# Kernel tuning notes

Hardware: AMD Instinct MI355X
Metric: run time of the kernel (lower is better)

## Reference

```python
import jax, jax.numpy as jnp
import numpy as np

# Module constants (from init_kwargs)
ANCHORS = np.array([[116.0, 90.0], [156.0, 198.0], [373.0, 326.0]], dtype=np.float32)
ANCHOR_AREAS = jnp.asarray(ANCHORS[:, 0] * ANCHORS[:, 1])  # [A]
A, H, W, C = 3, 128, 128, 2
IMG_W, IMG_H = 1024.0, 1024.0
STRIDE_W, STRIDE_H = IMG_W / H, IMG_H / W
ATTRS = 5 + C
LAMBDA_XY, LAMBDA_WH, LAMBDA_CONF, LAMBDA_CLS = 2.5, 2.5, 1.0, 1.0


def setup_inputs() -> dict:
    key = jax.random.key(0)
    k1, k2, k3, k4, k5 = jax.random.split(key, 5)
    B, T = 64, 2
    # conf/class feed BCELoss -> predictions must lie in [0,1)
    output = jax.random.uniform(k1, (B, A * H * W * ATTRS), dtype=jnp.float32)
    # Corner-format target boxes constructed so the (buggy) cell index
    # int((w - cx)/stride) is always within [0, mapSize).
    x1 = jax.random.uniform(k2, (B, T), minval=0.0, maxval=20.0)
    y1 = jax.random.uniform(k3, (B, T), minval=0.0, maxval=20.0)
    x2 = x1 + jax.random.uniform(k4, (B, T), minval=200.0, maxval=880.0)
    y2 = y1 + jax.random.uniform(k5, (B, T), minval=200.0, maxval=880.0)
    boxes = jnp.stack([x1, y1, x2, y2], axis=-1)  # [B,T,4]
    areas = (x2 - x1) * (y2 - y1)                 # [B,T]
    labels = jnp.ones((B, T), dtype=jnp.int32)    # label 1 -> valid for both one-hot quirks
    return {"output": output, "boxes": boxes, "labels": labels, "areas": areas}


def _bce(p, t):
    # torch BCELoss: mean, with log clamped to -100
    lp = jnp.maximum(jnp.log(p), -100.0)
    l1p = jnp.maximum(jnp.log1p(-p), -100.0)
    return -jnp.mean(t * lp + (1.0 - t) * l1p)


def _mse(p, t):
    return jnp.mean((p - t) ** 2)


def yolo_loss(output, boxes, labels, areas):
    B = output.shape[0]
    T = boxes.shape[1]
    out = output.reshape(B, A, H, W, ATTRS)
    x, y, w, h, conf = out[..., 0], out[..., 1], out[..., 2], out[..., 3], out[..., 4]
    cls = out[..., 5:]  # [B,A,H,W,C]

    gx = jnp.arange(H, dtype=output.dtype)[None, None, :, None]  # xCoord axis
    gy = jnp.arange(W, dtype=output.dtype)[None, None, None, :]  # yCoord axis
    x = x - gx
    y = y - gy

    # convert target boxes corners -> center format (done in-place in the original)
    cx = (boxes[..., 0] + boxes[..., 2]) * 0.5
    cy = (boxes[..., 1] + boxes[..., 3]) * 0.5
    bw = boxes[..., 2] - boxes[..., 0]
    bh = boxes[..., 3] - boxes[..., 1]
    tb = jnp.stack([cx, cy, bw, bh], axis=-1)  # [B,T,4]

    # class one-hots: target 0 uses labels[0]; targets i>=1 use labels[i]-1 (original quirk)
    cls0 = jax.nn.one_hot(labels[:, 0], C, dtype=output.dtype)
    cls1 = jax.nn.one_hot(labels[:, 1] - 1, C, dtype=output.dtype)
    tcls = jnp.stack([cls0, cls1], axis=1)            # [B,T,C]
    full = jnp.concatenate([tb, tcls], axis=-1)       # [B,T,4+C]

    best_anchor = jnp.argmin(jnp.abs(ANCHOR_AREAS[None, None, :] - areas[..., None]), axis=-1)  # [B,T]
    # original computes cell as int((w - cx)/stride), int((h - cy)/stride)
    cellX = ((bw - cx) / STRIDE_W).astype(jnp.int32)
    cellY = ((bh - cy) / STRIDE_H).astype(jnp.int32)

    mask = jnp.zeros((B, A, H, W), jnp.int32)
    exact = jnp.zeros((B, A, H, W), bool)
    bidx = jnp.arange(B)
    for i in range(T):  # tiny fixed loop over targets; later targets overwrite, as in torch
        mask = mask.at[bidx, best_anchor[:, i], cellX[:, i], cellY[:, i]].set(i)
        exact = exact.at[bidx, best_anchor[:, i], cellX[:, i], cellY[:, i]].set(True)

    matched = full[bidx[:, None, None, None], mask]  # [B,A,H,W,4+C]

    zero = jnp.zeros((), output.dtype)
    tX = jnp.where(exact, matched[..., 0] - gx, zero)
    tY = jnp.where(exact, matched[..., 1] - gy, zero)
    tW = jnp.where(exact, matched[..., 2], zero)
    tH = jnp.where(exact, matched[..., 3], zero)
    tConf = exact.astype(output.dtype)
    # targetMatched[5:] has length C-1==1 and broadcasts to all C slots (original quirk)
    tCls = jnp.where(exact[..., None], jnp.broadcast_to(matched[..., 5:6], cls.shape), zero)

    # IOU: prediction (x-gx, y-gy, w, h) converted center->corners; target center-format
    # boxes are (incorrectly, but faithfully) treated as corners.
    px1, py1 = x - w * 0.5, y - h * 0.5
    px2, py2 = x + w * 0.5, y + h * 0.5
    tx1 = tb[..., 0][:, None, None, None, :]  # [B,1,1,1,T]
    ty1 = tb[..., 1][:, None, None, None, :]
    tx2 = tb[..., 2][:, None, None, None, :]
    ty2 = tb[..., 3][:, None, None, None, :]
    ix = jnp.clip(jnp.minimum(px2[..., None], tx2) - jnp.maximum(px1[..., None], tx1), 0.0)
    iy = jnp.clip(jnp.minimum(py2[..., None], ty2) - jnp.maximum(py1[..., None], ty1), 0.0)
    inter = ix * iy                                   # [B,A,H,W,T]
    area_p = (px2 - px1) * (py2 - py1)                # [B,A,H,W]
    area_t = ((tx2 - tx1) * (ty2 - ty1))              # [B,1,1,1,T]
    iou = inter / (area_p[..., None] + area_t - inter + 1e-16)
    max_iou = jnp.max(iou, axis=-1)                   # [B,A,H,W]

    suppress = jnp.logical_and(~exact, max_iou > 0.5)
    xf = jnp.where(exact, x, zero)
    yf = jnp.where(exact, y, zero)
    wf = jnp.where(exact, w, zero)
    hf = jnp.where(exact, h, zero)
    clsf = jnp.where(exact[..., None], cls, zero)
    conff = jnp.where(suppress, zero, conf)

    xL, yL = _mse(xf, tX), _mse(yf, tY)
    wL, hL = _mse(wf, tW), _mse(hf, tH)
    confL = _bce(conff, tConf)
    clsL = _bce(clsf, tCls)
    loss = (xL + yL) * LAMBDA_XY + (wL + hL) * LAMBDA_WH + confL * LAMBDA_CONF + clsL * LAMBDA_CLS
    return (loss, xL, yL, wL, hL, confL, clsL)


def reference(output, boxes, labels, areas):
    return yolo_loss(output, boxes, labels, areas)
```

## Files before the change

### kernel.cpp

```cpp
#include <hip/hip_runtime.h>
#include <math.h>

#define A_ 3
#define H_ 128
#define W_ 128
#define C_ 2
#define ATTRS 7
#define B_ 64
#define CELLS_PER_BATCH (A_*H_*W_)
#define TOTAL_CELLS (B_*CELLS_PER_BATCH)

#define NTHR 256
#define CPT 4
#define CELLS_PER_BLOCK (NTHR*CPT)
#define NBLK (TOTAL_CELLS/CELLS_PER_BLOCK)

__global__ __launch_bounds__(NTHR) void yolo_main_k(
    const float* __restrict__ outp,
    const float* __restrict__ boxes,
    const int*   __restrict__ labels,
    const float* __restrict__ areas,
    float* __restrict__ ws)
{
    __shared__ float s_red[4][6];
    const int tid   = threadIdx.x;
    const int bcell = blockIdx.x * CELLS_PER_BLOCK;
    const int base  = bcell + tid * CPT;

    const int b = bcell / CELLS_PER_BATCH;

    float cxA[2], cyA[2], bwA[2], bhA[2], atA[2], t5A[2];
    int   baA[2], cXA[2], cYA[2];
    #pragma unroll
    for (int t = 0; t < 2; ++t) {
        const float x1 = boxes[b*8 + t*4 + 0];
        const float y1 = boxes[b*8 + t*4 + 1];
        const float x2 = boxes[b*8 + t*4 + 2];
        const float y2 = boxes[b*8 + t*4 + 3];
        const float cx = (x1 + x2) * 0.5f, cy = (y1 + y2) * 0.5f;
        const float bw = x2 - x1,          bh = y2 - y1;
        cxA[t] = cx; cyA[t] = cy; bwA[t] = bw; bhA[t] = bh;
        atA[t] = (bw - cx) * (bh - cy);
        const float ar = areas[b*2 + t];
        const float d0 = fabsf(10440.f - ar);
        const float d1 = fabsf(30888.f - ar);
        const float d2 = fabsf(121598.f - ar);
        int ba = 0; float bd = d0;
        if (d1 < bd) { ba = 1; bd = d1; }
        if (d2 < bd) { ba = 2; }
        baA[t] = ba;
        cXA[t] = (int)((bw - cx) * 0.125f);
        cYA[t] = (int)((bh - cy) * 0.125f);
        const int lab = labels[b*2 + t];
        t5A[t] = (t == 0) ? (lab == 1 ? 1.f : 0.f) : (lab == 2 ? 1.f : 0.f);
    }

    float f[28];
    const float4* gp = (const float4*)(outp + (size_t)base * ATTRS);
    #pragma unroll
    for (int m = 0; m < 7; ++m) ((float4*)f)[m] = gp[m];

    const int r  = base - b * CELLS_PER_BATCH;
    const int a  = r >> 14;
    const int i  = (r >> 7) & 127;
    const int j0 = r & 127;
    const float fi = (float)i;

    const bool ai0 = (a == baA[0]) && (i == cXA[0]);
    const bool ai1 = (a == baA[1]) && (i == cXA[1]);

    float accX = 0.f, accY = 0.f, accW = 0.f, accH = 0.f, accC = 0.f, accK = 0.f;

    #pragma unroll
    for (int k = 0; k < CPT; ++k) {
        const int   jj = j0 + k;
        const float fj = (float)jj;
        const float xr   = f[7*k+0], yr = f[7*k+1];
        const float w    = f[7*k+2], h  = f[7*k+3];
        const float conf = f[7*k+4], c0 = f[7*k+5], c1 = f[7*k+6];

        const float x = xr - fi, y = yr - fj;
        const float hw = 0.5f * w, hh = 0.5f * h;
        const float px1 = x - hw, px2 = x + hw;
        const float py1 = y - hh, py2 = y + hh;
        const float areaP = (px2 - px1) * (py2 - py1);

        bool e[2]; float iou[2];
        #pragma unroll
        for (int t = 0; t < 2; ++t) {
            e[t] = (t ? ai1 : ai0) && (jj == cYA[t]);
            const float ix = fmaxf(fminf(px2, bwA[t]) - fmaxf(px1, cxA[t]), 0.f);
            const float iy = fmaxf(fminf(py2, bhA[t]) - fmaxf(py1, cyA[t]), 0.f);
            const float in_ = ix * iy;
            iou[t] = in_ / (areaP + atA[t] - in_ + 1e-16f);
        }
        const bool  exact = e[0] || e[1];
        const float miou  = fmaxf(iou[0], iou[1]);
        const bool  suppress = (!exact) && (miou > 0.5f);

        if (exact) {
            const int t = e[1] ? 1 : 0;
            const float dx = x - (cxA[t] - fi); accX += dx * dx;
            const float dy = y - (cyA[t] - fj); accY += dy * dy;
            const float dw = w - bwA[t];        accW += dw * dw;
            const float dh = h - bhA[t];        accH += dh * dh;
            accC += fmaxf(logf(conf), -100.f);
            if (t5A[t] != 0.f)
                accK += fmaxf(logf(c0), -100.f) + fmaxf(logf(c1), -100.f);
            else
                accK += fmaxf(log1pf(-c0), -100.f) + fmaxf(log1pf(-c1), -100.f);
        } else if (!suppress) {
            accC += fmaxf(log1pf(-conf), -100.f);
        }
    }

    float v[6] = {accX, accY, accW, accH, accC, accK};
    #pragma unroll
    for (int m = 0; m < 6; ++m) {
        float s = v[m];
        #pragma unroll
        for (int off = 32; off > 0; off >>= 1) s += __shfl_down(s, off, 64);
        v[m] = s;
    }
    const int wid = tid >> 6;
    if ((tid & 63) == 0) {
        #pragma unroll
        for (int m = 0; m < 6; ++m) s_red[wid][m] = v[m];
    }
    __syncthreads();
    if (tid < 6) {
        const float s = s_red[0][tid] + s_red[1][tid] + s_red[2][tid] + s_red[3][tid];
        ws[tid * NBLK + blockIdx.x] = s;
    }
}

__global__ __launch_bounds__(384) void finalize_k(const float* __restrict__ ws,
                                                  float* __restrict__ o)
{
    __shared__ float s_fin[6];
    const int tid = threadIdx.x;
    const int m   = tid >> 6;
    const int l   = tid & 63;
    float s = 0.f;
    for (int k = l; k < NBLK; k += 64) s += ws[m * NBLK + k];
    #pragma unroll
    for (int off = 32; off > 0; off >>= 1) s += __shfl_down(s, off, 64);
    if (l == 0) s_fin[m] = s;
    __syncthreads();
    if (tid == 0) {
        const float N = (float)TOTAL_CELLS;
        const float xL = s_fin[0] / N, yL = s_fin[1] / N;
        const float wL = s_fin[2] / N, hL = s_fin[3] / N;
        const float confL = -s_fin[4] / N;
        const float clsL  = -s_fin[5] / (N * (float)C_);
        o[0] = 2.5f * (xL + yL) + 2.5f * (wL + hL) + confL + clsL;
        o[1] = xL; o[2] = yL; o[3] = wL; o[4] = hL; o[5] = confL; o[6] = clsL;
    }
}

extern "C" void kernel_launch(void* const* d_in, const int* in_sizes, int n_in,
                              void* d_out, int out_size, void* d_ws, size_t ws_size,
                              hipStream_t stream) {
    const float* outp   = (const float*)d_in[0];
    const float* boxes  = (const float*)d_in[1];
    const int*   labels = (const int*)d_in[2];
    const float* areas  = (const float*)d_in[3];
    float* ws = (float*)d_ws;
    float* o  = (float*)d_out;

    yolo_main_k<<<NBLK, NTHR, 0, stream>>>(outp, boxes, labels, areas, ws);
    finalize_k<<<1, 384, 0, stream>>>(ws, o);
}
```

Measured before the change: 149.1 us.

## Stage cell data through double-buffered LDS tiles with coalesced float4 loads

Replaces per-thread strided loads of 4 consecutive cells (7 float4 each) with block-wide coalesced float4 loads into a double-buffered shared-memory tile. Each thread then processes one cell per iteration across 8 iterations, with the next tile's loads issued before the current tile is computed. Blocks now cover 2048 cells, so there are half as many blocks and a smaller partial-sum workspace. The cost is a __syncthreads per iteration and LDS reads at stride 7 floats, and the loop now rests on a single barrier per iteration with the two LDS buffers alternating.

```diff
diff --git a/kernel.cpp b/kernel.cpp
--- a/kernel.cpp
+++ b/kernel.cpp
@@ -11,9 +11,10 @@
 #define TOTAL_CELLS (B_*CELLS_PER_BATCH)
 
 #define NTHR 256
-#define CPT 4
-#define CELLS_PER_BLOCK (NTHR*CPT)
+#define ITERS 8
+#define CELLS_PER_BLOCK (NTHR*ITERS)
 #define NBLK (TOTAL_CELLS/CELLS_PER_BLOCK)
+#define TILE_F4 448
 
 __global__ __launch_bounds__(NTHR) void yolo_main_k(
     const float* __restrict__ outp,
@@ -22,12 +23,11 @@
     const float* __restrict__ areas,
     float* __restrict__ ws)
 {
-    __shared__ float s_red[4][6];
+    __shared__ float4 s_tile[2][TILE_F4];
+    __shared__ float  s_red[4][6];
     const int tid   = threadIdx.x;
     const int bcell = blockIdx.x * CELLS_PER_BLOCK;
-    const int base  = bcell + tid * CPT;
-
-    const int b = bcell / CELLS_PER_BATCH;
+    const int b     = bcell / CELLS_PER_BATCH;
 
     float cxA[2], cyA[2], bwA[2], bhA[2], atA[2], t5A[2];
     int   baA[2], cXA[2], cYA[2];
@@ -55,29 +55,39 @@
         t5A[t] = (t == 0) ? (lab == 1 ? 1.f : 0.f) : (lab == 2 ? 1.f : 0.f);
     }
 
-    float f[28];
-    const float4* gp = (const float4*)(outp + (size_t)base * ATTRS);
-    #pragma unroll
-    for (int m = 0; m < 7; ++m) ((float4*)f)[m] = gp[m];
+    const int  rblk = bcell - b * CELLS_PER_BATCH;
+    const int  a    = rblk >> 14;
+    const bool aok0 = (a == baA[0]);
+    const bool aok1 = (a == baA[1]);
 
-    const int r  = base - b * CELLS_PER_BATCH;
-    const int a  = r >> 14;
-    const int i  = (r >> 7) & 127;
-    const int j0 = r & 127;
-    const float fi = (float)i;
-
-    const bool ai0 = (a == baA[0]) && (i == cXA[0]);
-    const bool ai1 = (a == baA[1]) && (i == cXA[1]);
+    const float4* g = (const float4*)(outp + (size_t)bcell * ATTRS);
+    float4 p0 = g[tid];
+    float4 p1;
+    if (tid < 192) p1 = g[tid + 256];
 
     float accX = 0.f, accY = 0.f, accW = 0.f, accH = 0.f, accC = 0.f, accK = 0.f;
+    int cur = 0;
 
-    #pragma unroll
-    for (int k = 0; k < CPT; ++k) {
-        const int   jj = j0 + k;
-        const float fj = (float)jj;
-        const float xr   = f[7*k+0], yr = f[7*k+1];
-        const float w    = f[7*k+2], h  = f[7*k+3];
-        const float conf = f[7*k+4], c0 = f[7*k+5], c1 = f[7*k+6];
+    for (int it = 0; it < ITERS; ++it) {
+        s_tile[cur][tid] = p0;
+        if (tid < 192) s_tile[cur][tid + 256] = p1;
+        __syncthreads();
+
+        if (it + 1 < ITERS) {
+            const float4* gn = g + (it + 1) * TILE_F4;
+            p0 = gn[tid];
+            if (tid < 192) p1 = gn[tid + 256];
+        }
+
+        const float* sp = ((const float*)s_tile[cur]) + tid * ATTRS;
+        const float xr   = sp[0], yr = sp[1];
+        const float w    = sp[2], h  = sp[3];
+        const float conf = sp[4], c0 = sp[5], c1 = sp[6];
+
+        const int r = rblk + it * NTHR + tid;
+        const int i = (r >> 7) & 127;
+        const int j = r & 127;
+        const float fi = (float)i, fj = (float)j;
 
         const float x = xr - fi, y = yr - fj;
         const float hw = 0.5f * w, hh = 0.5f * h;
@@ -88,7 +98,7 @@
         bool e[2]; float iou[2];
         #pragma unroll
         for (int t = 0; t < 2; ++t) {
-            e[t] = (t ? ai1 : ai0) && (jj == cYA[t]);
+            e[t] = (t ? aok1 : aok0) && (i == cXA[t]) && (j == cYA[t]);
             const float ix = fmaxf(fminf(px2, bwA[t]) - fmaxf(px1, cxA[t]), 0.f);
             const float iy = fmaxf(fminf(py2, bhA[t]) - fmaxf(py1, cyA[t]), 0.f);
             const float in_ = ix * iy;
@@ -112,6 +122,8 @@
         } else if (!suppress) {
             accC += fmaxf(log1pf(-conf), -100.f);
         }
+
+        cur ^= 1;
     }
 
     float v[6] = {accX, accY, accW, accH, accC, accK};
```

New measurement: 142.4 us. 1.05x faster.
